# Optimization experiments

Measured on AMD Instinct MI355X. Metric: run time of the kernel, lower is better.

## Reference

```python
import jax, jax.numpy as jnp
import numpy as np

N_AGENTS = 8
STATE_DIM = 256
EMBED_DIM = 32
BATCH = 65536


def setup_inputs() -> dict:
    key = jax.random.key(0)
    ks = jax.random.split(key, 12)
    s = 1.0 / np.sqrt(STATE_DIM)
    se = 1.0 / np.sqrt(EMBED_DIM)
    return {
        "agent_qs": jax.random.normal(ks[0], (BATCH, N_AGENTS), dtype=jnp.float32),
        "states": jax.random.normal(ks[1], (BATCH, STATE_DIM), dtype=jnp.float32),
        # hyper_w_1: Linear(state_dim, embed_dim * n_agents)
        "w1_W": jax.random.uniform(ks[2], (STATE_DIM, EMBED_DIM * N_AGENTS), jnp.float32, -s, s),
        "w1_b": jax.random.uniform(ks[3], (EMBED_DIM * N_AGENTS,), jnp.float32, -s, s),
        # hyper_w_final: Linear(state_dim, embed_dim)
        "wf_W": jax.random.uniform(ks[4], (STATE_DIM, EMBED_DIM), jnp.float32, -s, s),
        "wf_b": jax.random.uniform(ks[5], (EMBED_DIM,), jnp.float32, -s, s),
        # hyper_b_1: Linear(state_dim, embed_dim)
        "b1_W": jax.random.uniform(ks[6], (STATE_DIM, EMBED_DIM), jnp.float32, -s, s),
        "b1_b": jax.random.uniform(ks[7], (EMBED_DIM,), jnp.float32, -s, s),
        # V: Linear(state_dim, embed_dim) -> ReLU -> Linear(embed_dim, 1)
        "v1_W": jax.random.uniform(ks[8], (STATE_DIM, EMBED_DIM), jnp.float32, -s, s),
        "v1_b": jax.random.uniform(ks[9], (EMBED_DIM,), jnp.float32, -s, s),
        "v2_W": jax.random.uniform(ks[10], (EMBED_DIM, 1), jnp.float32, -se, se),
        "v2_b": jax.random.uniform(ks[11], (1,), jnp.float32, -se, se),
    }


def reference(agent_qs, states, w1_W, w1_b, wf_W, wf_b, b1_W, b1_b, v1_W, v1_b, v2_W, v2_b):
    B = agent_qs.shape[0]
    # hypernet weights (abs for monotonicity)
    w1 = jnp.abs(states @ w1_W + w1_b).reshape(B, N_AGENTS, EMBED_DIM)   # [B, A, E]
    w_final = jnp.abs(states @ wf_W + wf_b)                               # [B, E]
    b1 = states @ b1_W + b1_b                                             # [B, E]
    # hidden = elu(agent_qs^T w1 + b1): [B,1,A] @ [B,A,E] -> [B,E]
    hidden = jax.nn.elu(jnp.einsum("ba,bae->be", agent_qs, w1) + b1)
    # mixed = hidden @ w_final: [B,1,E] @ [B,E,1] -> [B,1]
    mixed = jnp.sum(hidden * w_final, axis=-1, keepdims=True)             # [B, 1]
    # state value V(s)
    state_value = jax.nn.relu(states @ v1_W + v1_b) @ v2_W + v2_b         # [B, 1]
    return mixed + state_value
```

## Files before the change

kernel.cpp:

```cpp
#include <hip/hip_runtime.h>
#include <math.h>


#define NTILES 22
#define KCHUNKS 8

typedef __attribute__((ext_vector_type(8))) short short8;
typedef __attribute__((ext_vector_type(4))) float float4v;

__device__ __forceinline__ unsigned short f2b(float f) {
    unsigned int u = __float_as_uint(f);
    u = u + 0x7fffu + ((u >> 16) & 1u);
    return (unsigned short)(u >> 16);
}

__global__ void repack_b(const float* __restrict__ w1_W,
                         const float* __restrict__ wf_W,
                         const float* __restrict__ b1_W,
                         const float* __restrict__ v1_W,
                         unsigned short* __restrict__ brep) {
    int idx = blockIdx.x * 256 + threadIdx.x;
    int lane = idx & 63;
    int tt   = idx >> 6;
    int tile = tt % 22;
    int kc   = tt / 22;
    int kbase = kc * 32 + (lane >> 4) * 8;
    int n = tile * 16 + (lane & 15);
    short8 frag;
#pragma unroll
    for (int j = 0; j < 8; ++j) {
        int k = kbase + j;
        float val;
        if (n < 256)      val = w1_W[k * 256 + n];
        else if (n < 288) val = wf_W[k * 32 + (n - 256)];
        else if (n < 320) val = b1_W[k * 32 + (n - 288)];
        else              val = v1_W[k * 32 + (n - 320)];
        frag[j] = (short)f2b(val);
    }
    *(short8*)(&brep[idx * 8]) = frag;
}

__global__ void __launch_bounds__(256, 3)
qmix_main(const float* __restrict__ agent_qs,
          const float* __restrict__ states,
          const unsigned short* __restrict__ brep,
          const float* __restrict__ w1_b,
          const float* __restrict__ wf_b,
          const float* __restrict__ b1_b,
          const float* __restrict__ v1_b,
          const float* __restrict__ v2_W,
          const float* __restrict__ v2_b,
          float* __restrict__ out) {
    const int tid  = threadIdx.x;
    const int wave = tid >> 6, lane = tid & 63;
    const int quad = lane >> 4, l16 = lane & 15;
    const int row  = blockIdx.x * 64 + wave * 16 + l16;
    const float* srow = states + (size_t)row * 256;

    short8 bfr[KCHUNKS];
#pragma unroll
    for (int kc = 0; kc < KCHUNKS; ++kc) {
        float4v a0 = *(const float4v*)(srow + kc * 32 + quad * 8);
        float4v a1 = *(const float4v*)(srow + kc * 32 + quad * 8 + 4);
        short8 bf;
#pragma unroll
        for (int j = 0; j < 4; ++j) {
            bf[j]     = (short)f2b(a0[j]);
            bf[4 + j] = (short)f2b(a1[j]);
        }
        bfr[kc] = bf;
    }

    float4v acc[NTILES];
#pragma unroll
    for (int t = 0; t < NTILES; ++t)
#pragma unroll
        for (int q = 0; q < 4; ++q) acc[t][q] = 0.f;

    for (int kc = 0; kc < KCHUNKS; ++kc) {
        const short8* ap = (const short8*)brep + kc * 1408 + lane;
        short8 bf = bfr[kc];
#pragma unroll
        for (int t = 0; t < NTILES; ++t) {
            short8 af = ap[t * 64];
            acc[t] = __builtin_amdgcn_mfma_f32_16x16x32_bf16(af, bf, acc[t], 0, 0, 0);
        }
    }

    float4v q0 = *(const float4v*)(agent_qs + (size_t)row * 8);
    float4v q1 = *(const float4v*)(agent_qs + (size_t)row * 8 + 4);
    float qv[8] = {q0[0], q0[1], q0[2], q0[3], q1[0], q1[1], q1[2], q1[3]};

    float qacc[8], wfv[8], b1v[8], svp = 0.f;
#pragma unroll
    for (int s = 0; s < 8; ++s) qacc[s] = 0.f;

#pragma unroll
    for (int t = 0; t < NTILES; ++t) {
        const float* bptr =
            (t < 16) ? (w1_b + t * 16) :
            (t < 18) ? (wf_b + (t - 16) * 16) :
            (t < 20) ? (b1_b + (t - 18) * 16) : (v1_b + (t - 20) * 16);
        float4v bb = *(const float4v*)(bptr + quad * 4);
        float vb[4];
#pragma unroll
        for (int j = 0; j < 4; ++j) vb[j] = acc[t][j] + bb[j];

        if (t < 16) {
            float q = qv[t >> 1];
            int base = (t & 1) * 4;
#pragma unroll
            for (int j = 0; j < 4; ++j) qacc[base + j] += q * fabsf(vb[j]);
        } else if (t < 18) {
            int base = (t - 16) * 4;
#pragma unroll
            for (int j = 0; j < 4; ++j) wfv[base + j] = fabsf(vb[j]);
        } else if (t < 20) {
            int base = (t - 18) * 4;
#pragma unroll
            for (int j = 0; j < 4; ++j) b1v[base + j] = vb[j];
        } else {
            int ebase = (t - 20) * 16 + quad * 4;
#pragma unroll
            for (int j = 0; j < 4; ++j)
                svp += fmaxf(vb[j], 0.f) * v2_W[ebase + j];
        }
    }

    float mix = 0.f;
#pragma unroll
    for (int s = 0; s < 8; ++s) {
        float h = qacc[s] + b1v[s];
        h = h > 0.f ? h : (__expf(h) - 1.f);
        mix += h * wfv[s];
    }
    float tot = mix + svp;
    tot += __shfl_xor(tot, 16);
    tot += __shfl_xor(tot, 32);
    if (quad == 0) out[row] = tot + v2_b[0];
}

extern "C" void kernel_launch(void* const* d_in, const int* in_sizes, int n_in,
                              void* d_out, int out_size, void* d_ws, size_t ws_size,
                              hipStream_t stream) {
    const float* agent_qs = (const float*)d_in[0];
    const float* states   = (const float*)d_in[1];
    const float* w1_W = (const float*)d_in[2];
    const float* w1_b = (const float*)d_in[3];
    const float* wf_W = (const float*)d_in[4];
    const float* wf_b = (const float*)d_in[5];
    const float* b1_W = (const float*)d_in[6];
    const float* b1_b = (const float*)d_in[7];
    const float* v1_W = (const float*)d_in[8];
    const float* v1_b = (const float*)d_in[9];
    const float* v2_W = (const float*)d_in[10];
    const float* v2_b = (const float*)d_in[11];
    float* out = (float*)d_out;
    unsigned short* brep = (unsigned short*)d_ws;

    repack_b<<<44, 256, 0, stream>>>(w1_W, wf_W, b1_W, v1_W, brep);
    qmix_main<<<1024, 256, 0, stream>>>(agent_qs, states, brep,
                                        w1_b, wf_b, b1_b, v1_b, v2_W, v2_b, out);
}
```

Measured before the change: 152.5 us.

## Process two row groups per wave and stage part of weights in LDS

Each wave now computes 32 rows instead of 16, so every weight fragment load feeds two MFMAs. The first 8 weight tiles are copied into shared memory per block, and the rest are still read from global/L2. The repack layout becomes tile-major to match, and the grid is halved. The cost is doubled accumulator registers (occupancy lowered to 1 block per SM in launch bounds), fewer waves to hide latency, and the LDS fill plus barrier at the start of each block.

```diff
diff --git a/kernel.cpp b/kernel.cpp
--- a/kernel.cpp
+++ b/kernel.cpp
@@ -4,9 +4,11 @@
 
 #define NTILES 22
 #define KCHUNKS 8
+#define LDS_T  8
 
 typedef __attribute__((ext_vector_type(8))) short short8;
 typedef __attribute__((ext_vector_type(4))) float float4v;
+typedef __attribute__((ext_vector_type(4))) int int4v;
 
 __device__ __forceinline__ unsigned short f2b(float f) {
     unsigned int u = __float_as_uint(f);
@@ -21,11 +23,11 @@
                          unsigned short* __restrict__ brep) {
     int idx = blockIdx.x * 256 + threadIdx.x;
     int lane = idx & 63;
-    int tt   = idx >> 6;
-    int tile = tt % 22;
-    int kc   = tt / 22;
+    int tk   = idx >> 6;
+    int t    = tk >> 3;
+    int kc   = tk & 7;
     int kbase = kc * 32 + (lane >> 4) * 8;
-    int n = tile * 16 + (lane & 15);
+    int n = t * 16 + (lane & 15);
     short8 frag;
 #pragma unroll
     for (int j = 0; j < 8; ++j) {
@@ -40,7 +42,7 @@
     *(short8*)(&brep[idx * 8]) = frag;
 }
 
-__global__ void __launch_bounds__(256, 3)
+__global__ void __launch_bounds__(256, 1)
 qmix_main(const float* __restrict__ agent_qs,
           const float* __restrict__ states,
           const unsigned short* __restrict__ brep,
@@ -51,93 +53,116 @@
           const float* __restrict__ v2_W,
           const float* __restrict__ v2_b,
           float* __restrict__ out) {
+    __shared__ __align__(16) unsigned short wlds[LDS_T * KCHUNKS * 64 * 8];
+
     const int tid  = threadIdx.x;
     const int wave = tid >> 6, lane = tid & 63;
     const int quad = lane >> 4, l16 = lane & 15;
-    const int row  = blockIdx.x * 64 + wave * 16 + l16;
-    const float* srow = states + (size_t)row * 256;
+    const int r0 = blockIdx.x * 128 + wave * 32 + l16;
 
-    short8 bfr[KCHUNKS];
+    short8 bfr[2][KCHUNKS];
 #pragma unroll
-    for (int kc = 0; kc < KCHUNKS; ++kc) {
-        float4v a0 = *(const float4v*)(srow + kc * 32 + quad * 8);
-        float4v a1 = *(const float4v*)(srow + kc * 32 + quad * 8 + 4);
-        short8 bf;
+    for (int g = 0; g < 2; ++g) {
+        const float* srow = states + (size_t)(r0 + g * 16) * 256;
 #pragma unroll
-        for (int j = 0; j < 4; ++j) {
-            bf[j]     = (short)f2b(a0[j]);
-            bf[4 + j] = (short)f2b(a1[j]);
-        }
-        bfr[kc] = bf;
-    }
-
-    float4v acc[NTILES];
+        for (int kc = 0; kc < KCHUNKS; ++kc) {
+            float4v a0 = *(const float4v*)(srow + kc * 32 + quad * 8);
+            float4v a1 = *(const float4v*)(srow + kc * 32 + quad * 8 + 4);
+            short8 bf;
 #pragma unroll
-    for (int t = 0; t < NTILES; ++t)
-#pragma unroll
-        for (int q = 0; q < 4; ++q) acc[t][q] = 0.f;
-
-    for (int kc = 0; kc < KCHUNKS; ++kc) {
-        const short8* ap = (const short8*)brep + kc * 1408 + lane;
-        short8 bf = bfr[kc];
-#pragma unroll
-        for (int t = 0; t < NTILES; ++t) {
-            short8 af = ap[t * 64];
-            acc[t] = __builtin_amdgcn_mfma_f32_16x16x32_bf16(af, bf, acc[t], 0, 0, 0);
+            for (int j = 0; j < 4; ++j) {
+                bf[j]     = (short)f2b(a0[j]);
+                bf[4 + j] = (short)f2b(a1[j]);
+            }
+            bfr[g][kc] = bf;
         }
     }
 
-    float4v q0 = *(const float4v*)(agent_qs + (size_t)row * 8);
-    float4v q1 = *(const float4v*)(agent_qs + (size_t)row * 8 + 4);
-    float qv[8] = {q0[0], q0[1], q0[2], q0[3], q1[0], q1[1], q1[2], q1[3]};
+    {
+        const int4v* src = (const int4v*)brep;
+        int4v* dst = (int4v*)wlds;
+#pragma unroll
+        for (int i = 0; i < 16; ++i)
+            dst[tid + i * 256] = src[tid + i * 256];
+    }
+    __syncthreads();
 
-    float qacc[8], wfv[8], b1v[8], svp = 0.f;
+    float4v acc[2][NTILES];
 #pragma unroll
-    for (int s = 0; s < 8; ++s) qacc[s] = 0.f;
+    for (int g = 0; g < 2; ++g)
+#pragma unroll
+        for (int t = 0; t < NTILES; ++t)
+#pragma unroll
+            for (int q = 0; q < 4; ++q) acc[g][t][q] = 0.f;
 
+    const short8* wl = (const short8*)wlds + lane;
+    const short8* ws = (const short8*)brep + lane;
 #pragma unroll
-    for (int t = 0; t < NTILES; ++t) {
-        const float* bptr =
-            (t < 16) ? (w1_b + t * 16) :
-            (t < 18) ? (wf_b + (t - 16) * 16) :
-            (t < 20) ? (b1_b + (t - 18) * 16) : (v1_b + (t - 20) * 16);
-        float4v bb = *(const float4v*)(bptr + quad * 4);
-        float vb[4];
+    for (int kc = 0; kc < KCHUNKS; ++kc) {
+        short8 b0 = bfr[0][kc], b1 = bfr[1][kc];
 #pragma unroll
-        for (int j = 0; j < 4; ++j) vb[j] = acc[t][j] + bb[j];
-
-        if (t < 16) {
-            float q = qv[t >> 1];
-            int base = (t & 1) * 4;
-#pragma unroll
-            for (int j = 0; j < 4; ++j) qacc[base + j] += q * fabsf(vb[j]);
-        } else if (t < 18) {
-            int base = (t - 16) * 4;
-#pragma unroll
-            for (int j = 0; j < 4; ++j) wfv[base + j] = fabsf(vb[j]);
-        } else if (t < 20) {
-            int base = (t - 18) * 4;
-#pragma unroll
-            for (int j = 0; j < 4; ++j) b1v[base + j] = vb[j];
-        } else {
-            int ebase = (t - 20) * 16 + quad * 4;
-#pragma unroll
-            for (int j = 0; j < 4; ++j)
-                svp += fmaxf(vb[j], 0.f) * v2_W[ebase + j];
+        for (int t = 0; t < NTILES; ++t) {
+            short8 af = (t < LDS_T) ? wl[(t * 8 + kc) * 64] : ws[(t * 8 + kc) * 64];
+            acc[0][t] = __builtin_amdgcn_mfma_f32_16x16x32_bf16(af, b0, acc[0][t], 0, 0, 0);
+            acc[1][t] = __builtin_amdgcn_mfma_f32_16x16x32_bf16(af, b1, acc[1][t], 0, 0, 0);
         }
     }
 
-    float mix = 0.f;
 #pragma unroll
-    for (int s = 0; s < 8; ++s) {
-        float h = qacc[s] + b1v[s];
-        h = h > 0.f ? h : (__expf(h) - 1.f);
-        mix += h * wfv[s];
+    for (int g = 0; g < 2; ++g) {
+        const int row = r0 + g * 16;
+        float4v q0 = *(const float4v*)(agent_qs + (size_t)row * 8);
+        float4v q1 = *(const float4v*)(agent_qs + (size_t)row * 8 + 4);
+        float qv[8] = {q0[0], q0[1], q0[2], q0[3], q1[0], q1[1], q1[2], q1[3]};
+
+        float qacc[8], wfv[8], b1v[8], svp = 0.f;
+#pragma unroll
+        for (int s = 0; s < 8; ++s) qacc[s] = 0.f;
+
+#pragma unroll
+        for (int t = 0; t < NTILES; ++t) {
+            const float* bptr =
+                (t < 16) ? (w1_b + t * 16) :
+                (t < 18) ? (wf_b + (t - 16) * 16) :
+                (t < 20) ? (b1_b + (t - 18) * 16) : (v1_b + (t - 20) * 16);
+            float4v bb = *(const float4v*)(bptr + quad * 4);
+            float vb[4];
+#pragma unroll
+            for (int j = 0; j < 4; ++j) vb[j] = acc[g][t][j] + bb[j];
+
+            if (t < 16) {
+                float q = qv[t >> 1];
+                int base = (t & 1) * 4;
+#pragma unroll
+                for (int j = 0; j < 4; ++j) qacc[base + j] += q * fabsf(vb[j]);
+            } else if (t < 18) {
+                int base = (t - 16) * 4;
+#pragma unroll
+                for (int j = 0; j < 4; ++j) wfv[base + j] = fabsf(vb[j]);
+            } else if (t < 20) {
+                int base = (t - 18) * 4;
+#pragma unroll
+                for (int j = 0; j < 4; ++j) b1v[base + j] = vb[j];
+            } else {
+                int ebase = (t - 20) * 16 + quad * 4;
+#pragma unroll
+                for (int j = 0; j < 4; ++j)
+                    svp += fmaxf(vb[j], 0.f) * v2_W[ebase + j];
+            }
+        }
+
+        float mix = 0.f;
+#pragma unroll
+        for (int s = 0; s < 8; ++s) {
+            float h = qacc[s] + b1v[s];
+            h = h > 0.f ? h : (__expf(h) - 1.f);
+            mix += h * wfv[s];
+        }
+        float tot = mix + svp;
+        tot += __shfl_xor(tot, 16);
+        tot += __shfl_xor(tot, 32);
+        if (quad == 0) out[row] = tot + v2_b[0];
     }
-    float tot = mix + svp;
-    tot += __shfl_xor(tot, 16);
-    tot += __shfl_xor(tot, 32);
-    if (quad == 0) out[row] = tot + v2_b[0];
 }
 
 extern "C" void kernel_launch(void* const* d_in, const int* in_sizes, int n_in,
@@ -159,6 +184,6 @@
     unsigned short* brep = (unsigned short*)d_ws;
 
     repack_b<<<44, 256, 0, stream>>>(w1_W, wf_W, b1_W, v1_W, brep);
-    qmix_main<<<1024, 256, 0, stream>>>(agent_qs, states, brep,
-                                        w1_b, wf_b, b1_b, v1_b, v2_W, v2_b, out);
+    qmix_main<<<512, 256, 0, stream>>>(agent_qs, states, brep,
+                                       w1_b, wf_b, b1_b, v1_b, v2_W, v2_b, out);
 }
```

After: 183.0 us. 1.2x slower.
